# Kernel tuning notes

Hardware: AMD Instinct MI355X
Metric: run time of the kernel (lower is better)

## Reference

```python
import jax, jax.numpy as jnp
import numpy as np

N = 50000        # n_nodes
E = 1_600_000    # n_edges (avg degree 32)
IN = 128         # in_dim
H = 8            # num_heads
R = 16           # hidden_rank
D = 16           # out_dim (per head)
SCALE = float(np.sqrt(D))


def setup_inputs() -> dict:
    key = jax.random.key(0)
    k1, k2, k3, k4, k5, k6 = jax.random.split(key, 6)
    h = jax.random.normal(k1, (N, IN), jnp.float32)
    src = jax.random.randint(k2, (E,), 0, N, dtype=jnp.int32)
    dst = jax.random.randint(k3, (E,), 0, N, dtype=jnp.int32)
    s = 1.0 / np.sqrt(IN)  # kaiming-ish scale
    p = jax.random.normal(k4, (IN, H * R), jnp.float32) * s
    q = jax.random.normal(k5, (IN, H * R), jnp.float32) * s
    Wv = jax.random.normal(k6, (IN, H * D), jnp.float32) * s
    return {"h": h, "src": src, "dst": dst, "p": p, "q": q, "Wv": Wv}


def reference(h, src, dst, p, q, Wv):
    # global_attention_type == 'transform' -> atted = h
    K = (h @ q).reshape(N, H, R)   # K_h = atted @ _q
    Q = (h @ p).reshape(N, H, R)   # Q_h = h @ _p
    V = (h @ Wv).reshape(N, H, D)  # V_h = V(h), no bias
    # per-edge score: (K[src] * Q[dst]).sum(-1, keepdim), then scaled exp
    score = jnp.sum(K[src] * Q[dst], axis=-1, keepdims=True)   # [E, H, 1]
    score = jnp.exp(jnp.clip(score / SCALE, -5.0, 5.0))
    # scatter-sum into destination nodes
    wV = jax.ops.segment_sum(V[src] * score, dst, num_segments=N)  # [N, H, D]
    z = jax.ops.segment_sum(score, dst, num_segments=N)            # [N, H, 1]
    z = jnp.where(z == 0, jnp.float32(0.001), z)
    return wV / z
```

## Files before the change

kernel.cpp:

```cpp
#include <hip/hip_runtime.h>
#include <hip/hip_fp16.h>


#define HNODE 64
#define EPB   8192
#define BKT_SHIFT 7
#define BKT_CAP 5120
#define CHUNK 64

typedef _Float16 f16x8 __attribute__((ext_vector_type(8)));
typedef float    f32x4 __attribute__((ext_vector_type(4)));
typedef _Float16 hv2   __attribute__((ext_vector_type(2)));

__device__ __forceinline__ float fdot2(unsigned a, unsigned b, float c) {
#if __has_builtin(__builtin_amdgcn_fdot2)
    return __builtin_amdgcn_fdot2(__builtin_bit_cast(hv2, a),
                                  __builtin_bit_cast(hv2, b), c, false);
#else
    __half2 ah = *(__half2*)&a, bh = *(__half2*)&b;
    float2 af = __half22float2(ah), bf = __half22float2(bh);
    return c + af.x * bf.x + af.y * bf.y;
#endif
}

__device__ __forceinline__ float2 h2f(unsigned u) {
    __half2 hh = *(__half2*)&u;
    return __half22float2(hh);
}

__device__ __forceinline__ unsigned pack2(float a, float b) {
    __half2 hh = __floats2half2_rn(a, b);
    return *(unsigned*)&hh;
}

__global__ __launch_bounds__(256) void scatter_wt_kernel(
    const int* __restrict__ src, const int* __restrict__ dst,
    const float* __restrict__ Wq, const float* __restrict__ Wp,
    const float* __restrict__ Wv, __half* __restrict__ Wt,
    unsigned* __restrict__ ebuf, int* __restrict__ cnts,
    int E, int nbkt, int nblk)
{
    __shared__ int cnt[512];
    __shared__ int lofs[512];
    __shared__ int ts[256];
    __shared__ int tot_sh;
    __shared__ unsigned long long sorted[EPB];

    int t = threadIdx.x;
    int blk = blockIdx.x;

    {
        int o = blk * 256 + t;
        if (o < 3 * 128 * 128) {
            int m = o >> 14, rem = o & 16383;
            int nn = rem >> 7, kk = rem & 127;
            const float* W = (m == 0) ? Wq : (m == 1) ? Wp : Wv;
            Wt[o] = __float2half(W[kk * 128 + nn]);
        }
    }

    for (int i = t; i < 512; i += 256) cnt[i] = 0;
    __syncthreads();

    int4 sv[8], dv[8], rk[8];
    int base = blk * EPB + t * 4;
    #pragma unroll
    for (int r = 0; r < 8; r++) {
        int i = base + r * 1024;
        if (i + 3 < E) {
            sv[r] = *(const int4*)(src + i);
            dv[r] = *(const int4*)(dst + i);
        } else {
            int tsrc[4], tdst[4];
            for (int k = 0; k < 4; k++) {
                int j = i + k;
                tsrc[k] = (j < E) ? src[j] : 0;
                tdst[k] = (j < E) ? dst[j] : -1;
            }
            sv[r] = make_int4(tsrc[0], tsrc[1], tsrc[2], tsrc[3]);
            dv[r] = make_int4(tdst[0], tdst[1], tdst[2], tdst[3]);
        }
        rk[r].x = (dv[r].x >= 0) ? atomicAdd(&cnt[dv[r].x >> BKT_SHIFT], 1) : 0;
        rk[r].y = (dv[r].y >= 0) ? atomicAdd(&cnt[dv[r].y >> BKT_SHIFT], 1) : 0;
        rk[r].z = (dv[r].z >= 0) ? atomicAdd(&cnt[dv[r].z >> BKT_SHIFT], 1) : 0;
        rk[r].w = (dv[r].w >= 0) ? atomicAdd(&cnt[dv[r].w >> BKT_SHIFT], 1) : 0;
    }
    __syncthreads();

    for (int i = t; i < nbkt; i += 256)
        cnts[blk * 512 + i] = cnt[i];

    int c0 = cnt[2 * t], c1 = cnt[2 * t + 1];
    int ps = c0 + c1;
    ts[t] = ps; __syncthreads();
    for (int off = 1; off < 256; off <<= 1) {
        int x = ts[t];
        int y = (t >= off) ? ts[t - off] : 0;
        __syncthreads();
        ts[t] = x + y;
        __syncthreads();
    }
    int pbase = ts[t] - ps;
    lofs[2 * t] = pbase;
    lofs[2 * t + 1] = pbase + c0;
    if (t == 255) tot_sh = ts[255];
    __syncthreads();

    #pragma unroll
    for (int r = 0; r < 8; r++) {
        int s, d;
        d = dv[r].x; if (d >= 0) { s = sv[r].x; sorted[lofs[d >> BKT_SHIFT] + rk[r].x] = ((unsigned long long)d << 18) | (unsigned)s; }
        d = dv[r].y; if (d >= 0) { s = sv[r].y; sorted[lofs[d >> BKT_SHIFT] + rk[r].y] = ((unsigned long long)d << 18) | (unsigned)s; }
        d = dv[r].z; if (d >= 0) { s = sv[r].z; sorted[lofs[d >> BKT_SHIFT] + rk[r].z] = ((unsigned long long)d << 18) | (unsigned)s; }
        d = dv[r].w; if (d >= 0) { s = sv[r].w; sorted[lofs[d >> BKT_SHIFT] + rk[r].w] = ((unsigned long long)d << 18) | (unsigned)s; }
    }
    __syncthreads();

    int tot = tot_sh;
    #pragma unroll
    for (int j = 0; j < 32; j++) {
        int i = j * 256 + t;
        if (i < tot) {
            unsigned long long e = sorted[i];
            int d = (int)(e >> 18);
            int b = d >> BKT_SHIFT;
            int k = i - lofs[b];
            if (k < CHUNK)
                ebuf[((size_t)b * nblk + blk) * CHUNK + k] =
                    ((unsigned)(d & 127) << 18) | (unsigned)(e & 0x3FFFFu);
        }
    }
}

__global__ __launch_bounds__(256) void gemm_kqv_kernel(
    const float* __restrict__ h, const __half* __restrict__ Wt,
    unsigned* __restrict__ KV, __half* __restrict__ Q, int n)
{
    __shared__ __align__(16) _Float16 ws[128 * 136];

    const int t = threadIdx.x;
    const int wid = t >> 6, lane = t & 63;
    const int node0 = blockIdx.x * HNODE;
    const int mrow = lane & 15, quad = lane >> 4;

    const int row = node0 + wid * 16 + mrow;
    const bool rowvalid = (row < n);
    const int rowc = rowvalid ? row : (n - 1);

    f16x8 hfr[4];
    #pragma unroll
    for (int s = 0; s < 4; s++) {
        const float4* hp = (const float4*)(h + (size_t)rowc * 128 + quad * 8 + 32 * s);
        float4 f0 = hp[0], f1 = hp[1];
        f16x8 a;
        a[0] = (_Float16)f0.x; a[1] = (_Float16)f0.y;
        a[2] = (_Float16)f0.z; a[3] = (_Float16)f0.w;
        a[4] = (_Float16)f1.x; a[5] = (_Float16)f1.y;
        a[6] = (_Float16)f1.z; a[7] = (_Float16)f1.w;
        hfr[s] = a;
    }

    f32x4 acc[3][8];
    #pragma unroll
    for (int m = 0; m < 3; m++)
        #pragma unroll
        for (int ct = 0; ct < 8; ct++) acc[m][ct] = (f32x4){0.f, 0.f, 0.f, 0.f};

    #pragma unroll
    for (int m = 0; m < 3; m++) {
        __syncthreads();
        {
            const uint4* wg = (const uint4*)(Wt + (size_t)m * 16384);
            #pragma unroll
            for (int i = 0; i < 8; i++) {
                int idx = t * 8 + i;
                int r = idx >> 4, seg = idx & 15;
                *(uint4*)(ws + r * 136 + seg * 8) = wg[idx];
            }
        }
        __syncthreads();
        #pragma unroll
        for (int s = 0; s < 4; s++) {
            #pragma unroll
            for (int ct = 0; ct < 8; ct++) {
                f16x8 a = *(const f16x8*)(ws + (ct * 16 + mrow) * 136 + quad * 8 + 32 * s);
                acc[m][ct] = __builtin_amdgcn_mfma_f32_16x16x32_f16(a, hfr[s], acc[m][ct], 0, 0, 0);
            }
        }
    }

    if (rowvalid) {
        unsigned* kvrow = KV + (size_t)row * 128;
        __half*   qrow  = Q  + (size_t)row * 128;
        #pragma unroll
        for (int ct = 0; ct < 8; ct++) {
            int qd = ct * 4 + quad;
            uint4 ov;
            ov.x = pack2(acc[0][ct][0], acc[0][ct][1]);
            ov.y = pack2(acc[0][ct][2], acc[0][ct][3]);
            ov.z = pack2(acc[2][ct][0], acc[2][ct][1]);
            ov.w = pack2(acc[2][ct][2], acc[2][ct][3]);
            *(uint4*)(kvrow + 4 * qd) = ov;
            uint2 qv;
            qv.x = pack2(acc[1][ct][0], acc[1][ct][1]);
            qv.y = pack2(acc[1][ct][2], acc[1][ct][3]);
            *(uint2*)(qrow + 4 * qd) = qv;
        }
    }
}

__global__ __launch_bounds__(1024) void fine_agg_kernel(
    const uint4* __restrict__ KV, const uint2* __restrict__ Qr,
    const unsigned* __restrict__ ebuf, const int* __restrict__ cnts,
    float4* __restrict__ out, int N, int nblk)
{
    __shared__ int cval[256];
    __shared__ int cofs[256];
    __shared__ int ts[256];
    __shared__ int ldeg[128];
    __shared__ int lstart[129];
    __shared__ int tot_sh;
    __shared__ unsigned sedge[BKT_CAP];
    __shared__ unsigned short srank[BKT_CAP];
    __shared__ int lcsr[BKT_CAP];

    int b = blockIdx.x, t = threadIdx.x;
    int node_base = b << BKT_SHIFT;

    if (t < 256) {
        int c = (t < nblk) ? cnts[t * 512 + b] : 0;
        if (c > CHUNK) c = CHUNK;
        cval[t] = c;
        ts[t] = c;
    }
    if (t < 128) ldeg[t] = 0;
    __syncthreads();
    for (int off = 1; off < 256; off <<= 1) {
        int x = (t < 256) ? ts[t] : 0;
        int y = (t >= off && t < 256) ? ts[t - off] : 0;
        __syncthreads();
        if (t < 256) ts[t] = x + y;
        __syncthreads();
    }
    if (t < 256) cofs[t] = ts[t] - cval[t];
    if (t == 255) tot_sh = ts[255] <= BKT_CAP ? ts[255] : BKT_CAP;
    __syncthreads();

    for (int idx = t; idx < nblk * CHUNK; idx += 1024) {
        int c = idx >> 6, k = idx & (CHUNK - 1);
        if (k < cval[c]) {
            int pos = cofs[c] + k;
            if (pos < BKT_CAP)
                sedge[pos] = ebuf[((size_t)b * nblk + c) * CHUNK + k];
        }
    }
    __syncthreads();

    int tot = tot_sh;
    for (int i = t; i < tot; i += 1024)
        srank[i] = (unsigned short)atomicAdd(&ldeg[sedge[i] >> 18], 1);
    __syncthreads();

    int mydeg = (t < 128) ? ldeg[t] : 0;
    if (t < 128) ts[t] = mydeg;
    __syncthreads();
    for (int off = 1; off < 128; off <<= 1) {
        int x = (t < 128) ? ts[t] : 0;
        int y = (t >= off && t < 128) ? ts[t - off] : 0;
        __syncthreads();
        if (t < 128) ts[t] = x + y;
        __syncthreads();
    }
    if (t < 128) lstart[t] = ts[t] - mydeg;
    if (t == 127) lstart[128] = ts[127];
    __syncthreads();

    for (int i = t; i < tot; i += 1024) {
        unsigned v = sedge[i];
        lcsr[lstart[v >> 18] + srank[i]] = (int)(v & 0x3FFFFu);
    }
    __syncthreads();

    int w = t >> 6, lane = t & 63;
    int l = lane & 31, eh = lane >> 5;
    for (int r = 0; r < 8; r++) {
        int nl = w * 8 + r;
        int node = node_base + nl;
        if (node >= N) break;
        int beg = lstart[nl], cnt = lstart[nl + 1] - beg;

        uint2 qq = Qr[(size_t)node * 32 + l];
        float4 accV = make_float4(0.f, 0.f, 0.f, 0.f);
        float accZ = 0.f;

        uint4 kvA = make_uint4(0, 0, 0, 0), kvB = make_uint4(0, 0, 0, 0);
        if (cnt > 0) kvA = KV[(size_t)lcsr[beg + ((eh < cnt) ? eh : 0)] * 32 + l];
        if (cnt > 2) kvB = KV[(size_t)lcsr[beg + ((2 + eh < cnt) ? 2 + eh : 0)] * 32 + l];

        for (int e = 0; e < cnt; e += 2) {
            uint4 nkv;
            bool more = (e + 4 < cnt);
            if (more) {
                int j = e + 4 + eh;
                if (j >= cnt) j = cnt - 1;
                nkv = KV[(size_t)lcsr[beg + j] * 32 + l];
            }
            float p = fdot2(kvA.x, qq.x, fdot2(kvA.y, qq.y, 0.f));
            p += __shfl_xor(p, 1);
            p += __shfl_xor(p, 2);
            float x = fminf(fmaxf(p * 0.25f, -5.f), 5.f);
            float sc = (e + eh < cnt) ? __expf(x) : 0.f;
            accZ += sc;
            float2 va = h2f(kvA.z), vb = h2f(kvA.w);
            accV.x += sc * va.x; accV.y += sc * va.y;
            accV.z += sc * vb.x; accV.w += sc * vb.y;
            kvA = kvB;
            if (more) kvB = nkv;
        }

        accZ   += __shfl_xor(accZ, 32);
        accV.x += __shfl_xor(accV.x, 32);
        accV.y += __shfl_xor(accV.y, 32);
        accV.z += __shfl_xor(accV.z, 32);
        accV.w += __shfl_xor(accV.w, 32);

        if (lane < 32) {
            if (accZ == 0.f) accZ = 0.001f;
            float inv = 1.0f / accZ;
            out[(size_t)node * 32 + l] =
                make_float4(accV.x * inv, accV.y * inv, accV.z * inv, accV.w * inv);
        }
    }
}


extern "C" void kernel_launch(void* const* d_in, const int* in_sizes, int n_in,
                              void* d_out, int out_size, void* d_ws, size_t ws_size,
                              hipStream_t stream)
{
    const float* h   = (const float*)d_in[0];
    const int*   src = (const int*)d_in[1];
    const int*   dst = (const int*)d_in[2];
    const float* p   = (const float*)d_in[3];
    const float* q   = (const float*)d_in[4];
    const float* wv  = (const float*)d_in[5];
    float* out = (float*)d_out;

    const int N = in_sizes[0] / 128;
    const int E = in_sizes[1];
    const int nbkt = (N + 127) >> BKT_SHIFT;
    const int nblk = (E + EPB - 1) / EPB;

    unsigned* KV = (unsigned*)d_ws;
    __half* Qh   = (__half*)(KV + (size_t)N * 128);
    unsigned* ebuf = (unsigned*)(Qh + (size_t)N * 128);
    int* cnts    = (int*)(ebuf + (size_t)nbkt * nblk * CHUNK);
    __half* Wt   = (__half*)(cnts + (size_t)nblk * 512);

    scatter_wt_kernel<<<nblk, 256, 0, stream>>>(src, dst, q, p, wv, Wt,
                                                ebuf, cnts, E, nbkt, nblk);

    gemm_kqv_kernel<<<(N + HNODE - 1) / HNODE, 256, 0, stream>>>(h, Wt, KV, Qh, N);

    fine_agg_kernel<<<nbkt, 1024, 0, stream>>>(
        (const uint4*)KV, (const uint2*)Qh, ebuf, cnts, (float4*)out, N, nblk);
}
```

Baseline: 253.1 us.

## Fuse edge bucketing with KQV GEMM and shrink buckets for finer aggregation

Merges the edge-scatter kernel and the KQV GEMM kernel into one launch whose blocks pick a role from their block index, so the two independent phases overlap and one launch is removed. The weight transpose to fp16 moves into each GEMM block, which reads fp32 weights directly instead of a pre-transposed buffer. Bucket size drops from 128 to 64 nodes with smaller edge chunks, and the aggregation kernel now uses 256-thread blocks and builds its local CSR with atomic cursors instead of staged rank arrays. Each GEMM block now converts and transposes the weights redundantly, and the smaller chunk and local capacities risk dropping edges for unusually dense buckets.

```diff
diff --git a/kernel.cpp b/kernel.cpp
--- a/kernel.cpp
+++ b/kernel.cpp
@@ -3,10 +3,10 @@
 
 
 #define HNODE 64
-#define EPB   8192
-#define BKT_SHIFT 7
-#define BKT_CAP 5120
-#define CHUNK 64
+#define EPB   4096
+#define BKT_SHIFT 6
+#define CHUNK 32
+#define LCAP  2816
 
 typedef _Float16 f16x8 __attribute__((ext_vector_type(8)));
 typedef float    f32x4 __attribute__((ext_vector_type(4)));
@@ -33,261 +33,249 @@
     return *(unsigned*)&hh;
 }
 
-__global__ __launch_bounds__(256) void scatter_wt_kernel(
+__global__ __launch_bounds__(256) void gemm_scatter_kernel(
+    const float* __restrict__ h,
+    const float* __restrict__ Wq, const float* __restrict__ Wp,
+    const float* __restrict__ Wv,
+    unsigned* __restrict__ KV, __half* __restrict__ Q, int n,
     const int* __restrict__ src, const int* __restrict__ dst,
-    const float* __restrict__ Wq, const float* __restrict__ Wp,
-    const float* __restrict__ Wv, __half* __restrict__ Wt,
     unsigned* __restrict__ ebuf, int* __restrict__ cnts,
-    int E, int nbkt, int nblk)
+    int E, int nbkt, int nblk_e)
 {
-    __shared__ int cnt[512];
-    __shared__ int lofs[512];
-    __shared__ int ts[256];
-    __shared__ int tot_sh;
-    __shared__ unsigned long long sorted[EPB];
-
-    int t = threadIdx.x;
-    int blk = blockIdx.x;
-
-    {
-        int o = blk * 256 + t;
-        if (o < 3 * 128 * 128) {
-            int m = o >> 14, rem = o & 16383;
-            int nn = rem >> 7, kk = rem & 127;
-            const float* W = (m == 0) ? Wq : (m == 1) ? Wp : Wv;
-            Wt[o] = __float2half(W[kk * 128 + nn]);
-        }
-    }
-
-    for (int i = t; i < 512; i += 256) cnt[i] = 0;
-    __syncthreads();
-
-    int4 sv[8], dv[8], rk[8];
-    int base = blk * EPB + t * 4;
-    #pragma unroll
-    for (int r = 0; r < 8; r++) {
-        int i = base + r * 1024;
-        if (i + 3 < E) {
-            sv[r] = *(const int4*)(src + i);
-            dv[r] = *(const int4*)(dst + i);
-        } else {
-            int tsrc[4], tdst[4];
-            for (int k = 0; k < 4; k++) {
-                int j = i + k;
-                tsrc[k] = (j < E) ? src[j] : 0;
-                tdst[k] = (j < E) ? dst[j] : -1;
-            }
-            sv[r] = make_int4(tsrc[0], tsrc[1], tsrc[2], tsrc[3]);
-            dv[r] = make_int4(tdst[0], tdst[1], tdst[2], tdst[3]);
-        }
-        rk[r].x = (dv[r].x >= 0) ? atomicAdd(&cnt[dv[r].x >> BKT_SHIFT], 1) : 0;
-        rk[r].y = (dv[r].y >= 0) ? atomicAdd(&cnt[dv[r].y >> BKT_SHIFT], 1) : 0;
-        rk[r].z = (dv[r].z >= 0) ? atomicAdd(&cnt[dv[r].z >> BKT_SHIFT], 1) : 0;
-        rk[r].w = (dv[r].w >= 0) ? atomicAdd(&cnt[dv[r].w >> BKT_SHIFT], 1) : 0;
-    }
-    __syncthreads();
-
-    for (int i = t; i < nbkt; i += 256)
-        cnts[blk * 512 + i] = cnt[i];
-
-    int c0 = cnt[2 * t], c1 = cnt[2 * t + 1];
-    int ps = c0 + c1;
-    ts[t] = ps; __syncthreads();
-    for (int off = 1; off < 256; off <<= 1) {
-        int x = ts[t];
-        int y = (t >= off) ? ts[t - off] : 0;
-        __syncthreads();
-        ts[t] = x + y;
-        __syncthreads();
-    }
-    int pbase = ts[t] - ps;
-    lofs[2 * t] = pbase;
-    lofs[2 * t + 1] = pbase + c0;
-    if (t == 255) tot_sh = ts[255];
-    __syncthreads();
-
-    #pragma unroll
-    for (int r = 0; r < 8; r++) {
-        int s, d;
-        d = dv[r].x; if (d >= 0) { s = sv[r].x; sorted[lofs[d >> BKT_SHIFT] + rk[r].x] = ((unsigned long long)d << 18) | (unsigned)s; }
-        d = dv[r].y; if (d >= 0) { s = sv[r].y; sorted[lofs[d >> BKT_SHIFT] + rk[r].y] = ((unsigned long long)d << 18) | (unsigned)s; }
-        d = dv[r].z; if (d >= 0) { s = sv[r].z; sorted[lofs[d >> BKT_SHIFT] + rk[r].z] = ((unsigned long long)d << 18) | (unsigned)s; }
-        d = dv[r].w; if (d >= 0) { s = sv[r].w; sorted[lofs[d >> BKT_SHIFT] + rk[r].w] = ((unsigned long long)d << 18) | (unsigned)s; }
-    }
-    __syncthreads();
-
-    int tot = tot_sh;
-    #pragma unroll
-    for (int j = 0; j < 32; j++) {
-        int i = j * 256 + t;
-        if (i < tot) {
-            unsigned long long e = sorted[i];
-            int d = (int)(e >> 18);
-            int b = d >> BKT_SHIFT;
-            int k = i - lofs[b];
-            if (k < CHUNK)
-                ebuf[((size_t)b * nblk + blk) * CHUNK + k] =
-                    ((unsigned)(d & 127) << 18) | (unsigned)(e & 0x3FFFFu);
-        }
-    }
-}
-
-__global__ __launch_bounds__(256) void gemm_kqv_kernel(
-    const float* __restrict__ h, const __half* __restrict__ Wt,
-    unsigned* __restrict__ KV, __half* __restrict__ Q, int n)
-{
-    __shared__ __align__(16) _Float16 ws[128 * 136];
-
+    __shared__ __align__(16) char smem[42240];
     const int t = threadIdx.x;
-    const int wid = t >> 6, lane = t & 63;
-    const int node0 = blockIdx.x * HNODE;
-    const int mrow = lane & 15, quad = lane >> 4;
-
-    const int row = node0 + wid * 16 + mrow;
-    const bool rowvalid = (row < n);
-    const int rowc = rowvalid ? row : (n - 1);
-
-    f16x8 hfr[4];
-    #pragma unroll
-    for (int s = 0; s < 4; s++) {
-        const float4* hp = (const float4*)(h + (size_t)rowc * 128 + quad * 8 + 32 * s);
-        float4 f0 = hp[0], f1 = hp[1];
-        f16x8 a;
-        a[0] = (_Float16)f0.x; a[1] = (_Float16)f0.y;
-        a[2] = (_Float16)f0.z; a[3] = (_Float16)f0.w;
-        a[4] = (_Float16)f1.x; a[5] = (_Float16)f1.y;
-        a[6] = (_Float16)f1.z; a[7] = (_Float16)f1.w;
-        hfr[s] = a;
-    }
-
-    f32x4 acc[3][8];
-    #pragma unroll
-    for (int m = 0; m < 3; m++)
-        #pragma unroll
-        for (int ct = 0; ct < 8; ct++) acc[m][ct] = (f32x4){0.f, 0.f, 0.f, 0.f};
-
-    #pragma unroll
-    for (int m = 0; m < 3; m++) {
-        __syncthreads();
-        {
-            const uint4* wg = (const uint4*)(Wt + (size_t)m * 16384);
+
+    if ((int)blockIdx.x >= nblk_e) {
+        _Float16* ws = (_Float16*)smem;
+        const int gblk = blockIdx.x - nblk_e;
+        const int wid = t >> 6, lane = t & 63;
+        const int node0 = gblk * HNODE;
+        const int mrow = lane & 15, quad = lane >> 4;
+
+        const int row = node0 + wid * 16 + mrow;
+        const bool rowvalid = (row < n);
+        const int rowc = rowvalid ? row : (n - 1);
+
+        f16x8 hfr[4];
+        #pragma unroll
+        for (int s = 0; s < 4; s++) {
+            const float4* hp = (const float4*)(h + (size_t)rowc * 128 + quad * 8 + 32 * s);
+            float4 f0 = hp[0], f1 = hp[1];
+            f16x8 a;
+            a[0] = (_Float16)f0.x; a[1] = (_Float16)f0.y;
+            a[2] = (_Float16)f0.z; a[3] = (_Float16)f0.w;
+            a[4] = (_Float16)f1.x; a[5] = (_Float16)f1.y;
+            a[6] = (_Float16)f1.z; a[7] = (_Float16)f1.w;
+            hfr[s] = a;
+        }
+
+        f32x4 acc[3][8];
+        #pragma unroll
+        for (int m = 0; m < 3; m++)
             #pragma unroll
-            for (int i = 0; i < 8; i++) {
-                int idx = t * 8 + i;
-                int r = idx >> 4, seg = idx & 15;
-                *(uint4*)(ws + r * 136 + seg * 8) = wg[idx];
-            }
-        }
-        __syncthreads();
-        #pragma unroll
-        for (int s = 0; s < 4; s++) {
+            for (int ct = 0; ct < 8; ct++) acc[m][ct] = (f32x4){0.f, 0.f, 0.f, 0.f};
+
+        const float* Ws[3] = {Wq, Wp, Wv};
+
+        #pragma unroll
+        for (int m = 0; m < 3; m++) {
+            __syncthreads();
+            {
+                const float* __restrict__ W = Ws[m];
+                for (int i = 0; i < 8; i++) {
+                    #pragma unroll
+                    for (int j = 0; j < 8; j++) {
+                        int idx = (i * 8 + j) * 256 + t;
+                        int kk = idx >> 7, nn = idx & 127;
+                        ws[nn * 136 + kk] = (_Float16)W[idx];
+                    }
+                }
+            }
+            __syncthreads();
+            #pragma unroll
+            for (int s = 0; s < 4; s++) {
+                #pragma unroll
+                for (int ct = 0; ct < 8; ct++) {
+                    f16x8 a = *(const f16x8*)(ws + (ct * 16 + mrow) * 136 + quad * 8 + 32 * s);
+                    acc[m][ct] = __builtin_amdgcn_mfma_f32_16x16x32_f16(a, hfr[s], acc[m][ct], 0, 0, 0);
+                }
+            }
+        }
+
+        if (rowvalid) {
+            unsigned* kvrow = KV + (size_t)row * 128;
+            __half*   qrow  = Q  + (size_t)row * 128;
             #pragma unroll
             for (int ct = 0; ct < 8; ct++) {
-                f16x8 a = *(const f16x8*)(ws + (ct * 16 + mrow) * 136 + quad * 8 + 32 * s);
-                acc[m][ct] = __builtin_amdgcn_mfma_f32_16x16x32_f16(a, hfr[s], acc[m][ct], 0, 0, 0);
-            }
-        }
-    }
-
-    if (rowvalid) {
-        unsigned* kvrow = KV + (size_t)row * 128;
-        __half*   qrow  = Q  + (size_t)row * 128;
-        #pragma unroll
-        for (int ct = 0; ct < 8; ct++) {
-            int qd = ct * 4 + quad;
-            uint4 ov;
-            ov.x = pack2(acc[0][ct][0], acc[0][ct][1]);
-            ov.y = pack2(acc[0][ct][2], acc[0][ct][3]);
-            ov.z = pack2(acc[2][ct][0], acc[2][ct][1]);
-            ov.w = pack2(acc[2][ct][2], acc[2][ct][3]);
-            *(uint4*)(kvrow + 4 * qd) = ov;
-            uint2 qv;
-            qv.x = pack2(acc[1][ct][0], acc[1][ct][1]);
-            qv.y = pack2(acc[1][ct][2], acc[1][ct][3]);
-            *(uint2*)(qrow + 4 * qd) = qv;
-        }
-    }
-}
-
-__global__ __launch_bounds__(1024) void fine_agg_kernel(
+                int qd = ct * 4 + quad;
+                uint4 ov;
+                ov.x = pack2(acc[0][ct][0], acc[0][ct][1]);
+                ov.y = pack2(acc[0][ct][2], acc[0][ct][3]);
+                ov.z = pack2(acc[2][ct][0], acc[2][ct][1]);
+                ov.w = pack2(acc[2][ct][2], acc[2][ct][3]);
+                *(uint4*)(kvrow + 4 * qd) = ov;
+                uint2 qv;
+                qv.x = pack2(acc[1][ct][0], acc[1][ct][1]);
+                qv.y = pack2(acc[1][ct][2], acc[1][ct][3]);
+                *(uint2*)(qrow + 4 * qd) = qv;
+            }
+        }
+    } else {
+        unsigned long long* sorted = (unsigned long long*)smem;
+        int* cnt    = (int*)(smem + 32768);
+        int* lofs   = (int*)(smem + 36864);
+        int* ts     = (int*)(smem + 40960);
+        int* tot_sh = (int*)(smem + 41984);
+
+        int blk = blockIdx.x;
+        for (int i = t; i < 1024; i += 256) cnt[i] = 0;
+        __syncthreads();
+
+        int4 sv[4], dv[4], rk[4];
+        int base = blk * EPB + t * 4;
+        #pragma unroll
+        for (int r = 0; r < 4; r++) {
+            int i = base + r * 1024;
+            if (i + 3 < E) {
+                sv[r] = *(const int4*)(src + i);
+                dv[r] = *(const int4*)(dst + i);
+            } else {
+                int tsrc[4], tdst[4];
+                for (int k = 0; k < 4; k++) {
+                    int j = i + k;
+                    tsrc[k] = (j < E) ? src[j] : 0;
+                    tdst[k] = (j < E) ? dst[j] : -1;
+                }
+                sv[r] = make_int4(tsrc[0], tsrc[1], tsrc[2], tsrc[3]);
+                dv[r] = make_int4(tdst[0], tdst[1], tdst[2], tdst[3]);
+            }
+            rk[r].x = (dv[r].x >= 0) ? atomicAdd(&cnt[dv[r].x >> BKT_SHIFT], 1) : 0;
+            rk[r].y = (dv[r].y >= 0) ? atomicAdd(&cnt[dv[r].y >> BKT_SHIFT], 1) : 0;
+            rk[r].z = (dv[r].z >= 0) ? atomicAdd(&cnt[dv[r].z >> BKT_SHIFT], 1) : 0;
+            rk[r].w = (dv[r].w >= 0) ? atomicAdd(&cnt[dv[r].w >> BKT_SHIFT], 1) : 0;
+        }
+        __syncthreads();
+
+        for (int i = t; i < nbkt; i += 256)
+            cnts[blk * 1024 + i] = cnt[i];
+
+        int c0 = cnt[4 * t], c1 = cnt[4 * t + 1], c2 = cnt[4 * t + 2], c3 = cnt[4 * t + 3];
+        int ps = c0 + c1 + c2 + c3;
+        ts[t] = ps; __syncthreads();
+        for (int off = 1; off < 256; off <<= 1) {
+            int x = ts[t];
+            int y = (t >= off) ? ts[t - off] : 0;
+            __syncthreads();
+            ts[t] = x + y;
+            __syncthreads();
+        }
+        int pb = ts[t] - ps;
+        lofs[4 * t] = pb;
+        lofs[4 * t + 1] = pb + c0;
+        lofs[4 * t + 2] = pb + c0 + c1;
+        lofs[4 * t + 3] = pb + c0 + c1 + c2;
+        if (t == 255) *tot_sh = ts[255];
+        __syncthreads();
+
+        #pragma unroll
+        for (int r = 0; r < 4; r++) {
+            int s, d;
+            d = dv[r].x; if (d >= 0) { s = sv[r].x; sorted[lofs[d >> BKT_SHIFT] + rk[r].x] = ((unsigned long long)d << 18) | (unsigned)s; }
+            d = dv[r].y; if (d >= 0) { s = sv[r].y; sorted[lofs[d >> BKT_SHIFT] + rk[r].y] = ((unsigned long long)d << 18) | (unsigned)s; }
+            d = dv[r].z; if (d >= 0) { s = sv[r].z; sorted[lofs[d >> BKT_SHIFT] + rk[r].z] = ((unsigned long long)d << 18) | (unsigned)s; }
+            d = dv[r].w; if (d >= 0) { s = sv[r].w; sorted[lofs[d >> BKT_SHIFT] + rk[r].w] = ((unsigned long long)d << 18) | (unsigned)s; }
+        }
+        __syncthreads();
+
+        int tot = *tot_sh;
+        #pragma unroll
+        for (int j = 0; j < 16; j++) {
+            int i = j * 256 + t;
+            if (i < tot) {
+                unsigned long long e = sorted[i];
+                int d = (int)(e >> 18);
+                int b = d >> BKT_SHIFT;
+                int k = i - lofs[b];
+                if (k < CHUNK)
+                    ebuf[((size_t)b * nblk_e + blk) * CHUNK + k] =
+                        ((unsigned)(d & 63) << 18) | (unsigned)(e & 0x3FFFFu);
+            }
+        }
+    }
+}
+
+__global__ __launch_bounds__(256) void fine_agg_kernel(
     const uint4* __restrict__ KV, const uint2* __restrict__ Qr,
     const unsigned* __restrict__ ebuf, const int* __restrict__ cnts,
-    float4* __restrict__ out, int N, int nblk)
+    float4* __restrict__ out, int N, int nblk_e)
 {
-    __shared__ int cval[256];
-    __shared__ int cofs[256];
+    __shared__ int cval[512];
     __shared__ int ts[256];
-    __shared__ int ldeg[128];
-    __shared__ int lstart[129];
-    __shared__ int tot_sh;
-    __shared__ unsigned sedge[BKT_CAP];
-    __shared__ unsigned short srank[BKT_CAP];
-    __shared__ int lcsr[BKT_CAP];
+    __shared__ int ldeg[64];
+    __shared__ int lcur[64];
+    __shared__ int lstart[65];
+    __shared__ int lcsr[LCAP];
 
     int b = blockIdx.x, t = threadIdx.x;
     int node_base = b << BKT_SHIFT;
 
-    if (t < 256) {
-        int c = (t < nblk) ? cnts[t * 512 + b] : 0;
-        if (c > CHUNK) c = CHUNK;
-        cval[t] = c;
-        ts[t] = c;
-    }
-    if (t < 128) ldeg[t] = 0;
-    __syncthreads();
-    for (int off = 1; off < 256; off <<= 1) {
-        int x = (t < 256) ? ts[t] : 0;
-        int y = (t >= off && t < 256) ? ts[t - off] : 0;
-        __syncthreads();
-        if (t < 256) ts[t] = x + y;
-        __syncthreads();
-    }
-    if (t < 256) cofs[t] = ts[t] - cval[t];
-    if (t == 255) tot_sh = ts[255] <= BKT_CAP ? ts[255] : BKT_CAP;
-    __syncthreads();
-
-    for (int idx = t; idx < nblk * CHUNK; idx += 1024) {
-        int c = idx >> 6, k = idx & (CHUNK - 1);
+    int c0 = (2 * t < nblk_e) ? cnts[(size_t)(2 * t) * 1024 + b] : 0;
+    int c1 = (2 * t + 1 < nblk_e) ? cnts[(size_t)(2 * t + 1) * 1024 + b] : 0;
+    if (c0 > CHUNK) c0 = CHUNK;
+    if (c1 > CHUNK) c1 = CHUNK;
+    cval[2 * t] = c0;
+    cval[2 * t + 1] = c1;
+    if (t < 64) ldeg[t] = 0;
+    __syncthreads();
+
+    int niter = nblk_e * CHUNK;
+    for (int idx = t; idx < niter; idx += 256) {
+        int c = idx >> 5, k = idx & 31;
         if (k < cval[c]) {
-            int pos = cofs[c] + k;
-            if (pos < BKT_CAP)
-                sedge[pos] = ebuf[((size_t)b * nblk + c) * CHUNK + k];
-        }
-    }
-    __syncthreads();
-
-    int tot = tot_sh;
-    for (int i = t; i < tot; i += 1024)
-        srank[i] = (unsigned short)atomicAdd(&ldeg[sedge[i] >> 18], 1);
-    __syncthreads();
-
-    int mydeg = (t < 128) ? ldeg[t] : 0;
-    if (t < 128) ts[t] = mydeg;
-    __syncthreads();
-    for (int off = 1; off < 128; off <<= 1) {
-        int x = (t < 128) ? ts[t] : 0;
-        int y = (t >= off && t < 128) ? ts[t - off] : 0;
-        __syncthreads();
-        if (t < 128) ts[t] = x + y;
-        __syncthreads();
-    }
-    if (t < 128) lstart[t] = ts[t] - mydeg;
-    if (t == 127) lstart[128] = ts[127];
-    __syncthreads();
-
-    for (int i = t; i < tot; i += 1024) {
-        unsigned v = sedge[i];
-        lcsr[lstart[v >> 18] + srank[i]] = (int)(v & 0x3FFFFu);
+            unsigned v = ebuf[((size_t)b * nblk_e + c) * CHUNK + k];
+            atomicAdd(&ldeg[v >> 18], 1);
+        }
+    }
+    __syncthreads();
+
+    int mydeg = (t < 64) ? ldeg[t] : 0;
+    if (t < 64) ts[t] = mydeg;
+    __syncthreads();
+    for (int off = 1; off < 64; off <<= 1) {
+        int x = (t < 64) ? ts[t] : 0;
+        int y = (t >= off && t < 64) ? ts[t - off] : 0;
+        __syncthreads();
+        if (t < 64) ts[t] = x + y;
+        __syncthreads();
+    }
+    if (t < 64) {
+        int lbeg = ts[t] - mydeg;
+        lstart[t] = lbeg;
+        lcur[t] = lbeg;
+    }
+    if (t == 63) lstart[64] = ts[63];
+    __syncthreads();
+
+    for (int idx = t; idx < niter; idx += 256) {
+        int c = idx >> 5, k = idx & 31;
+        if (k < cval[c]) {
+            unsigned v = ebuf[((size_t)b * nblk_e + c) * CHUNK + k];
+            int pos = atomicAdd(&lcur[v >> 18], 1);
+            if (pos < LCAP) lcsr[pos] = (int)(v & 0x3FFFFu);
+        }
     }
     __syncthreads();
 
     int w = t >> 6, lane = t & 63;
     int l = lane & 31, eh = lane >> 5;
-    for (int r = 0; r < 8; r++) {
-        int nl = w * 8 + r;
+    for (int r = 0; r < 16; r++) {
+        int nl = w * 16 + r;
         int node = node_base + nl;
         if (node >= N) break;
-        int beg = lstart[nl], cnt = lstart[nl + 1] - beg;
+        int beg = lstart[nl], end = lstart[nl + 1];
+        if (beg > LCAP) beg = LCAP;
+        if (end > LCAP) end = LCAP;
+        int cnt = end - beg;
 
         uint2 qq = Qr[(size_t)node * 32 + l];
         float4 accV = make_float4(0.f, 0.f, 0.f, 0.f);
@@ -348,20 +336,18 @@
 
     const int N = in_sizes[0] / 128;
     const int E = in_sizes[1];
-    const int nbkt = (N + 127) >> BKT_SHIFT;
-    const int nblk = (E + EPB - 1) / EPB;
+    const int nbkt = (N + 63) >> BKT_SHIFT;
+    const int nblk_e = (E + EPB - 1) / EPB;
+    const int gemm_blocks = (N + HNODE - 1) / HNODE;
 
     unsigned* KV = (unsigned*)d_ws;
     __half* Qh   = (__half*)(KV + (size_t)N * 128);
     unsigned* ebuf = (unsigned*)(Qh + (size_t)N * 128);
-    int* cnts    = (int*)(ebuf + (size_t)nbkt * nblk * CHUNK);
-    __half* Wt   = (__half*)(cnts + (size_t)nblk * 512);
-
-    scatter_wt_kernel<<<nblk, 256, 0, stream>>>(src, dst, q, p, wv, Wt,
-                                                ebuf, cnts, E, nbkt, nblk);
-
-    gemm_kqv_kernel<<<(N + HNODE - 1) / HNODE, 256, 0, stream>>>(h, Wt, KV, Qh, N);
-
-    fine_agg_kernel<<<nbkt, 1024, 0, stream>>>(
-        (const uint4*)KV, (const uint2*)Qh, ebuf, cnts, (float4*)out, N, nblk);
-}
+    int* cnts    = (int*)(ebuf + (size_t)nbkt * nblk_e * CHUNK);
+
+    gemm_scatter_kernel<<<nblk_e + gemm_blocks, 256, 0, stream>>>(
+        h, q, p, wv, KV, Qh, N, src, dst, ebuf, cnts, E, nbkt, nblk_e);
+
+    fine_agg_kernel<<<nbkt, 256, 0, stream>>>(
+        (const uint4*)KV, (const uint2*)Qh, ebuf, cnts, (float4*)out, N, nblk_e);
+}
```

New measurement: 283.2 us. 11.9% more time.
